# Kernel optimization log

Hardware: AMD Instinct MI355X
Metric: run time of the kernel (lower is better)

Reference implementation:

```python
import jax, jax.numpy as jnp
import numpy as np

E = 1024
H = 16
D = E // H  # head dim 64
B = 2
S = 2048


def setup_inputs() -> dict:
    key = jax.random.key(0)
    k1, k2, k3, k4, k5 = jax.random.split(key, 5)
    scale = 1.0 / np.sqrt(E)
    return {
        "x": jax.random.normal(k1, (B, S, E), dtype=jnp.float32),
        "W_in": jax.random.normal(k2, (E, 3 * E), dtype=jnp.float32) * scale,
        "b_in": jnp.zeros((3 * E,), dtype=jnp.float32),
        "W_out": jax.random.normal(k3, (E, E), dtype=jnp.float32) * scale,
        "b_out": jnp.zeros((E,), dtype=jnp.float32),
        "causal_mask": 1,
    }


def reference(x, W_in, b_in, W_out, b_out, causal_mask):
    b, s, e = x.shape
    qkv = x @ W_in + b_in                      # [B,S,3E]
    q, k, v = jnp.split(qkv, 3, axis=-1)
    # [B,S,E] -> [B,H,S,D]
    q = q.reshape(b, s, H, D).transpose(0, 2, 1, 3)
    k = k.reshape(b, s, H, D).transpose(0, 2, 1, 3)
    v = v.reshape(b, s, H, D).transpose(0, 2, 1, 3)
    scores = jnp.einsum("bhqd,bhkd->bhqk", q, k)
    if causal_mask:
        # mask applied before scaling in the original; -inf is scale-invariant
        mask = jnp.triu(jnp.ones((s, s), dtype=bool), k=1)
        scores = jnp.where(mask, -jnp.inf, scores)
    scores = scores / np.sqrt(D)
    weight = jax.nn.softmax(scores, axis=-1)
    out = jnp.einsum("bhqk,bhkd->bhqd", weight, v)   # [B,H,S,D]
    out = out.transpose(0, 2, 1, 3).reshape(b, s, e)
    return out @ W_out + b_out
```

## Files before the change

### kernel.cpp

```cpp
#include <hip/hip_runtime.h>
#include <hip/hip_bf16.h>
#include <cmath>

typedef __bf16 bf16;
typedef __attribute__((ext_vector_type(8))) __bf16 bf16x8;
typedef __attribute__((ext_vector_type(4))) __bf16 bf16x4;
typedef __attribute__((ext_vector_type(4))) float f32x4;
typedef __attribute__((ext_vector_type(16))) float f32x16;
typedef unsigned int u32;

constexpr int S  = 2048;
constexpr int E  = 1024;
constexpr int H  = 16;
constexpr int D  = 64;
constexpr int B  = 2;
constexpr int M  = B * S;
constexpr int N3 = 3 * E;
constexpr int NROWS = B * H * S;

__constant__ int P_tab_d[16] = {1,1,1,1,1,2,2,2,2,2,2,3,3,3,3,3};
__constant__ int S_tab_d[16] = {0,1,2,3,4,5,7,9,11,13,15,17,20,23,26,29};
__constant__ int c_ord_d[32] = {15,15,10,10, 15,14,14,14,13,9,9,4,
                                13,13,12,12,8,8, 12,11,11,11,7,7,3,
                                6,6, 5,5,2, 1, 0};
__constant__ int p_ord_d[32] = {1,2,0,1, 0,0,1,2,2,0,1,0,
                                0,1,1,2,0,1, 0,0,1,2,0,1,0,
                                0,1, 0,1,0, 0, 0};

static __device__ __forceinline__ void gload16(const void* g, void* l) {
  __builtin_amdgcn_global_load_lds((const __attribute__((address_space(1))) void*)g,
                                   (__attribute__((address_space(3))) void*)l, 16, 0, 0);
}

static __device__ __forceinline__ u32 pack2(float a, float b) {
  union { bf16 h[2]; u32 u; } r;
  r.h[0] = (bf16)a; r.h[1] = (bf16)b;
  return r.u;
}
typedef union { u32 w[4]; bf16x8 v; } FU;

__global__ __launch_bounds__(256) void k_prep(
    const float* __restrict__ x, bf16* __restrict__ xb,
    const float* __restrict__ W_in, bf16* __restrict__ wtin,
    const float* __restrict__ W_out, bf16* __restrict__ wtout)
{
  const int bid = blockIdx.x;
  if (bid < 4096) {
    const int i = (bid * 256 + threadIdx.x) * 4;
    const float4 v = *(const float4*)(x + i);
    bf16x4 o = { (bf16)v.x, (bf16)v.y, (bf16)v.z, (bf16)v.w };
    *(bf16x4*)(xb + i) = o;
  } else {
    __shared__ float t[32][33];
    const float* in;
    bf16* out;
    int R, C, bx, by;
    if (bid < 4096 + 3072) {
      const int b = bid - 4096;
      in = W_in; out = wtin; R = E; C = N3;
      bx = b % (N3 / 32); by = b / (N3 / 32);
    } else {
      const int b = bid - 4096 - 3072;
      in = W_out; out = wtout; R = E; C = E;
      bx = b % (E / 32); by = b / (E / 32);
    }
    const int c0 = bx * 32, r0 = by * 32;
    const int tx = threadIdx.x & 31, ty = threadIdx.x >> 5;
    #pragma unroll
    for (int j = 0; j < 32; j += 8)
      t[ty + j][tx] = in[(size_t)(r0 + ty + j) * C + c0 + tx];
    __syncthreads();
    #pragma unroll
    for (int j = 0; j < 32; j += 8)
      out[(size_t)(c0 + ty + j) * R + r0 + tx] = (bf16)t[tx][ty + j];
  }
}

template<int EPI>
__global__ __launch_bounds__(256) void k_gemm(
    const bf16* __restrict__ A, const bf16* __restrict__ Bt,
    const float* __restrict__ bias, float* __restrict__ outF,
    bf16* __restrict__ oQ, bf16* __restrict__ oK, bf16* __restrict__ oV,
    int Kdim, int Nn)
{
  __shared__ __align__(16) char smem[65536];
  const int tid = threadIdx.x;
  const int lane = tid & 63, w = tid >> 6;
  const int lane15 = lane & 15, quad = lane >> 4;
  const int wm = w >> 1, wn = w & 1;

  const int nbx = Nn >> 7;
  const int nwg = gridDim.x;
  const int bid = blockIdx.x;
  const int swz = (bid & 7) * (nwg >> 3) + (bid >> 3);
  const int bn0 = (swz % nbx) * 128;
  const int bm0 = (swz / nbx) * 128;

  const int so0 = w * 1024 + lane * 16;
  int srow[4], slk[4];
  #pragma unroll
  for (int p = 0; p < 4; ++p) {
    const int o = p * 4096 + so0;
    const int row = o >> 7, cbyte = o & 127;
    srow[p] = row;
    slk[p] = (cbyte ^ ((row & 7) << 4)) >> 1;
  }

  f32x4 acc[4][4] = {};
  const int nkt = Kdim >> 6;

  #pragma unroll
  for (int p = 0; p < 4; ++p) {
    gload16(A  + (size_t)(bm0 + srow[p]) * Kdim + slk[p], smem +         p * 4096 + w * 1024);
    gload16(Bt + (size_t)(bn0 + srow[p]) * Kdim + slk[p], smem + 32768 + p * 4096 + w * 1024);
  }

  #pragma unroll 1
  for (int kt = 0; kt < nkt; ++kt) {
    const int cur = kt & 1;
    __builtin_amdgcn_s_barrier();
    if (kt + 1 < nkt) {
      const int k0 = (kt + 1) << 6;
      const int nb = (cur ^ 1) * 16384;
      #pragma unroll
      for (int p = 0; p < 4; ++p) {
        gload16(A  + (size_t)(bm0 + srow[p]) * Kdim + k0 + slk[p],
                smem + nb +         p * 4096 + w * 1024);
        gload16(Bt + (size_t)(bn0 + srow[p]) * Kdim + k0 + slk[p],
                smem + nb + 32768 + p * 4096 + w * 1024);
      }
      asm volatile("s_waitcnt vmcnt(8)" ::: "memory");
    } else {
      asm volatile("s_waitcnt vmcnt(0)" ::: "memory");
    }
    __builtin_amdgcn_s_barrier();

    const char* cA = smem + cur * 16384;
    const char* cB = smem + 32768 + cur * 16384;
    #pragma unroll
    for (int kk = 0; kk < 2; ++kk) {
      bf16x8 af[4], bfr[4];
      #pragma unroll
      for (int f = 0; f < 4; ++f) {
        const int ra = wm * 64 + f * 16 + lane15;
        af[f] = *(const bf16x8*)(cA + ra * 128 +
                 ((kk * 64 + (quad << 4)) ^ ((ra & 7) << 4)));
        const int rb = wn * 64 + f * 16 + lane15;
        bfr[f] = *(const bf16x8*)(cB + rb * 128 +
                 ((kk * 64 + (quad << 4)) ^ ((rb & 7) << 4)));
      }
      #pragma unroll
      for (int i = 0; i < 4; ++i)
        #pragma unroll
        for (int j = 0; j < 4; ++j)
          acc[i][j] = __builtin_amdgcn_mfma_f32_16x16x32_bf16(af[i], bfr[j], acc[i][j], 0, 0, 0);
    }
  }

  if constexpr (EPI == 1) {
    #pragma unroll
    for (int i = 0; i < 4; ++i)
      #pragma unroll
      for (int j = 0; j < 4; ++j) {
        const int n = bn0 + wn * 64 + j * 16 + lane15;
        const float bv = bias[n];
        #pragma unroll
        for (int r = 0; r < 4; ++r) {
          const int m = bm0 + wm * 64 + i * 16 + quad * 4 + r;
          outF[(size_t)m * E + n] = acc[i][j][r] + bv;
        }
      }
  } else {
    const int which = bn0 >> 10;
    const int b  = bm0 >> 11;
    const int s0 = bm0 & (S - 1);
    const int cn0 = bn0 & (E - 1);
    if (which < 2) {
      __builtin_amdgcn_s_barrier();
      char* lC = smem;
      #pragma unroll
      for (int j = 0; j < 4; ++j) {
        const int n_loc = wn * 64 + j * 16 + lane15;
        const float bv = bias[bn0 + n_loc];
        #pragma unroll
        for (int i = 0; i < 4; ++i)
          #pragma unroll
          for (int r = 0; r < 4; ++r) {
            const int m_loc = wm * 64 + i * 16 + quad * 4 + r;
            *(bf16*)(lC + m_loc * 256 + ((n_loc * 2) ^ ((m_loc & 7) << 4))) =
                (bf16)(acc[i][j][r] + bv);
          }
      }
      __builtin_amdgcn_s_barrier();
      const int h0 = cn0 >> 6;
      #pragma unroll
      for (int it = 0; it < 8; ++it) {
        const int cch = w * 64 + it * 8 + (lane >> 3);
        const int m_loc = cch >> 1, hh = cch & 1, piece = lane & 7;
        const bf16x8 vv = *(const bf16x8*)(lC + m_loc * 256 +
                          ((hh * 128 + piece * 16) ^ ((m_loc & 7) << 4)));
        if (which == 0) {
          *(bf16x8*)(oQ + ((size_t)(b * H + h0 + hh) * S + s0 + m_loc) * D + piece * 8) = vv;
        } else {
          const size_t hb = (size_t)(b * H + h0 + hh) * S * D;
          const int tile = (s0 + m_loc) >> 6;
          const int row = m_loc & 63;
          *(bf16x8*)(oK + hb + (size_t)tile * 4096 + (piece >> 1) * 1024 +
                     (row >> 5) * 512 + (32 * (piece & 1) + (row & 31)) * 8) = vv;
        }
      }
    } else {
      #pragma unroll
      for (int j = 0; j < 4; ++j) {
        const int n_loc = wn * 64 + j * 16 + lane15;
        const int cn = cn0 + n_loc;
        const int hv = cn >> 6, dd = cn & 63;
        const float bv = bias[bn0 + n_loc];
        const size_t hb = (size_t)(b * H + hv) * S * D;
        #pragma unroll
        for (int i = 0; i < 4; ++i) {
          const int scol_g = s0 + wm * 64 + i * 16 + quad * 4;
          const int vtile = scol_g >> 6;
          const int cg = (scol_g & 63) >> 3;
          bf16x4 pk = { (bf16)(acc[i][j][0] + bv), (bf16)(acc[i][j][1] + bv),
                        (bf16)(acc[i][j][2] + bv), (bf16)(acc[i][j][3] + bv) };
          *(bf16x4*)(oV + hb + (size_t)vtile * 4096 + (cg >> 1) * 1024 +
                     (dd >> 5) * 512 + (32 * (cg & 1) + (dd & 31)) * 8 +
                     (quad & 1) * 4) = pk;
        }
      }
    }
  }
}

__global__ __launch_bounds__(256, 4) void k_attn(
    const bf16* __restrict__ Qb, const bf16* __restrict__ Kf, const bf16* __restrict__ Vf,
    bf16* __restrict__ pO0, bf16* __restrict__ pO1,
    float* __restrict__ pM, float* __restrict__ pL, const int* __restrict__ cmask)
{
  __shared__ float corr_lds[4][32];
  __shared__ float lrow_lds[4][32];

  const int tid = threadIdx.x, lane = tid & 63, w = tid >> 6;
  const int h = lane >> 5, q31 = lane & 31;
  const int bh = blockIdx.x;
  const int yy = blockIdx.y;
  const int c  = c_ord_d[yy];
  const int p  = p_ord_d[yy];
  const int Pc = P_tab_d[c];
  const int sslot = S_tab_d[c] + p;
  const int causal = cmask[0];
  const float S2 = 0.18033688011112042f;

  const bf16* Qh = Qb + (size_t)bh * S * D;
  const bf16* Kh = Kf + (size_t)bh * S * D;
  const bf16* Vh = Vf + (size_t)bh * S * D;

  const int nt = causal ? (2 * c + 2) : (S / 64);
  const int t0 = (p * nt) / Pc;
  const int t1 = ((p + 1) * nt) / Pc;
  const int q0w = c * 128 + 32 * w;
  const int qg  = q0w + q31;
  const int t1w = causal ? min(t1, ((q0w + 31) >> 6) + 1) : t1;

  bf16x8 qf[4];
  #pragma unroll
  for (int ds = 0; ds < 4; ++ds)
    qf[ds] = *(const bf16x8*)(Qh + (size_t)qg * D + 16 * ds + 8 * h);

  f32x16 o0 = {}, o1 = {};
  float mrun = -INFINITY, lr = 0.f;

  #pragma unroll 1
  for (int t = t0; t < t1w; ++t) {
    const bf16* ktb = Kh + (size_t)t * 4096;
    const bf16* vtb = Vh + (size_t)t * 4096;

    bf16x8 kf0[4], kf1[4];
    #pragma unroll
    for (int ds = 0; ds < 4; ++ds) {
      kf0[ds] = *(const bf16x8*)(ktb + ds * 1024 +       lane * 8);
      kf1[ds] = *(const bf16x8*)(ktb + ds * 1024 + 512 + lane * 8);
    }

    f32x16 s0v = {}, s1v = {};
    __builtin_amdgcn_s_setprio(1);
    #pragma unroll
    for (int ds = 0; ds < 4; ++ds) {
      s0v = __builtin_amdgcn_mfma_f32_32x32x16_bf16(kf0[ds], qf[ds], s0v, 0, 0, 0);
      s1v = __builtin_amdgcn_mfma_f32_32x32x16_bf16(kf1[ds], qf[ds], s1v, 0, 0, 0);
    }
    __builtin_amdgcn_s_setprio(0);

    if (causal && (64 * t + 63 > q0w)) {
      #pragma unroll
      for (int rr = 0; rr < 16; ++rr) {
        const int kg = 64 * t + (rr & 3) + 8 * (rr >> 2) + 4 * h;
        if (kg > qg)      s0v[rr] = -INFINITY;
        if (kg + 32 > qg) s1v[rr] = -INFINITY;
      }
    }

    float a8[8];
    #pragma unroll
    for (int i = 0; i < 8; ++i)
      a8[i] = fmaxf(fmaxf(s0v[i], s0v[i + 8]), fmaxf(s1v[i], s1v[i + 8]));
    float tmax = fmaxf(fmaxf(fmaxf(a8[0], a8[1]), fmaxf(a8[2], a8[3])),
                       fmaxf(fmaxf(a8[4], a8[5]), fmaxf(a8[6], a8[7])));
    tmax = fmaxf(tmax, __shfl_xor(tmax, 32, 64));

    const bool nogrow = __all(tmax <= mrun + 64.f);
    const float mnew = nogrow ? mrun : fmaxf(mrun, tmax);
    float corrf = 1.f;
    if (!nogrow) {
      corrf = __builtin_amdgcn_exp2f((mrun - mnew) * S2);
      corr_lds[w][q31] = corrf;
    }
    const float msc = mnew * S2;

    #pragma unroll
    for (int rr = 0; rr < 16; ++rr) {
      s0v[rr] = __builtin_amdgcn_exp2f(__builtin_fmaf(s0v[rr], S2, -msc));
      s1v[rr] = __builtin_amdgcn_exp2f(__builtin_fmaf(s1v[rr], S2, -msc));
    }

    float b8[8];
    #pragma unroll
    for (int i = 0; i < 8; ++i)
      b8[i] = (s0v[i] + s0v[i + 8]) + (s1v[i] + s1v[i + 8]);
    float psum = ((b8[0] + b8[1]) + (b8[2] + b8[3])) + ((b8[4] + b8[5]) + (b8[6] + b8[7]));
    psum += __shfl_xor(psum, 32, 64);
    lr = lr * corrf + psum;
    mrun = mnew;

    u32 pk[8][2];
    #pragma unroll
    for (int jj = 0; jj < 4; ++jj) {
      pk[jj][0]     = pack2(s0v[4 * jj],     s0v[4 * jj + 1]);
      pk[jj][1]     = pack2(s0v[4 * jj + 2], s0v[4 * jj + 3]);
      pk[jj + 4][0] = pack2(s1v[4 * jj],     s1v[4 * jj + 1]);
      pk[jj + 4][1] = pack2(s1v[4 * jj + 2], s1v[4 * jj + 3]);
    }

    if (!nogrow) {
      #pragma unroll
      for (int j = 0; j < 4; ++j) {
        const f32x4 cv = *(const f32x4*)&corr_lds[w][8 * j + 4 * h];
        #pragma unroll
        for (int sr = 0; sr < 4; ++sr) {
          o0[4 * j + sr] *= cv[sr];
          o1[4 * j + sr] *= cv[sr];
        }
      }
    }

    __builtin_amdgcn_s_setprio(1);
    #pragma unroll
    for (int ks = 0; ks < 4; ++ks) {
      u32 a0 = pk[2 * ks][0], b0 = pk[2 * ks + 1][0];
      u32 a1 = pk[2 * ks][1], b1 = pk[2 * ks + 1][1];
      asm volatile("v_permlane32_swap_b32 %0, %1" : "+v"(a0), "+v"(b0));
      asm volatile("v_permlane32_swap_b32 %0, %1" : "+v"(a1), "+v"(b1));
      FU f; f.w[0] = a0; f.w[1] = a1; f.w[2] = b0; f.w[3] = b1;
      const bf16x8 vf0 = *(const bf16x8*)(vtb + ks * 1024 +       lane * 8);
      const bf16x8 vf1 = *(const bf16x8*)(vtb + ks * 1024 + 512 + lane * 8);
      o0 = __builtin_amdgcn_mfma_f32_32x32x16_bf16(f.v, vf0, o0, 0, 0, 0);
      o1 = __builtin_amdgcn_mfma_f32_32x32x16_bf16(f.v, vf1, o1, 0, 0, 0);
    }
    __builtin_amdgcn_s_setprio(0);
  }

  const int slotbase = ((bh & 15) * 32 + sslot) * 128;
  if (h == 0) {
    pM[(size_t)(bh * 32 + sslot) * 128 + 32 * w + q31] = mrun;
    pL[(size_t)(bh * 32 + sslot) * 128 + 32 * w + q31] = lr;
  }
  lrow_lds[w][q31] = lr;
  bf16* po = (bh < 16 ? pO0 : pO1) + (size_t)slotbase * D;
  #pragma unroll
  for (int j = 0; j < 4; ++j) {
    const f32x4 lv = *(const f32x4*)&lrow_lds[w][8 * j + 4 * h];
    #pragma unroll
    for (int sr = 0; sr < 4; ++sr) {
      const int rr = 4 * j + sr;
      const float inv = lv[sr] > 0.f ? 1.0f / lv[sr] : 0.f;
      const int qloc = 32 * w + (rr & 3) + 8 * (rr >> 2) + 4 * h;
      bf16* dst = po + (size_t)qloc * D;
      dst[q31]      = (bf16)(o0[rr] * inv);
      dst[32 + q31] = (bf16)(o1[rr] * inv);
    }
  }
}

__global__ __launch_bounds__(256) void k_combine(
    const bf16* __restrict__ pO0, const bf16* __restrict__ pO1,
    const float* __restrict__ pM, const float* __restrict__ pL,
    bf16* __restrict__ AO)
{
  const float S2 = 0.18033688011112042f;
  const int idx = blockIdx.x * 256 + threadIdx.x;
  const int row = idx >> 3, d0 = (idx & 7) * 8;
  const int bh = row >> 11, s = row & 2047;
  const int c = s >> 7, local = s & 127;
  const int Pc = P_tab_d[c], Sc = S_tab_d[c];
  const bf16* pbase = (bh < 16 ? pO0 : pO1);

  float mv[3], lv[3];
  float m = -INFINITY;
  #pragma unroll
  for (int p = 0; p < 3; ++p) {
    if (p < Pc) {
      mv[p] = pM[(size_t)(bh * 32 + Sc + p) * 128 + local];
      lv[p] = pL[(size_t)(bh * 32 + Sc + p) * 128 + local];
      m = fmaxf(m, mv[p]);
    }
  }
  float wsum = 0.f, wv[3];
  #pragma unroll
  for (int p = 0; p < 3; ++p) {
    wv[p] = 0.f;
    if (p < Pc && lv[p] > 0.f) {
      wv[p] = lv[p] * __builtin_amdgcn_exp2f((mv[p] - m) * S2);
      wsum += wv[p];
    }
  }
  const float inv = 1.0f / wsum;
  float acc[8] = {};
  #pragma unroll
  for (int p = 0; p < 3; ++p) {
    if (p < Pc) {
      const bf16x8 a = *(const bf16x8*)(pbase +
          ((size_t)((bh & 15) * 32 + Sc + p) * 128 + local) * D + d0);
      #pragma unroll
      for (int i = 0; i < 8; ++i)
        acc[i] += wv[p] * (float)a[i];
    }
  }
  bf16x8 o;
  #pragma unroll
  for (int i = 0; i < 8; ++i)
    o[i] = (bf16)(acc[i] * inv);
  const int bb = row >> 15, hh = (row >> 11) & 15;
  *(bf16x8*)(AO + ((size_t)(bb * S + s)) * E + hh * D + d0) = o;
}

extern "C" void kernel_launch(void* const* d_in, const int* in_sizes, int n_in,
                              void* d_out, int out_size, void* d_ws, size_t ws_size,
                              hipStream_t stream) {
  (void)in_sizes; (void)n_in; (void)out_size; (void)ws_size;
  const float* x     = (const float*)d_in[0];
  const float* W_in  = (const float*)d_in[1];
  const float* b_in  = (const float*)d_in[2];
  const float* W_out = (const float*)d_in[3];
  const float* b_out = (const float*)d_in[4];
  const int*   cmask = (const int*)d_in[5];

  char* ws = (char*)d_ws;
  bf16* xb    = (bf16*)ws; ws += (size_t)M * E * 2;
  bf16* wtin  = (bf16*)ws; ws += (size_t)N3 * E * 2;
  bf16* wtout = (bf16*)ws; ws += (size_t)E * E * 2;
  bf16* qB    = (bf16*)ws; ws += (size_t)B * H * S * D * 2;
  bf16* kF    = (bf16*)ws; ws += (size_t)B * H * S * D * 2;
  bf16* vF    = (bf16*)ws; ws += (size_t)B * H * S * D * 2;
  bf16* ao    = (bf16*)ws; ws += (size_t)M * E * 2;
  bf16* pO1   = (bf16*)ws; ws += (size_t)NROWS * D * 2;
  float* pMb  = (float*)ws; ws += (size_t)2 * NROWS * 4;
  float* pLb  = (float*)ws; ws += (size_t)2 * NROWS * 4;
  bf16* pO0   = xb;

  k_prep<<<4096 + 3072 + 1024, 256, 0, stream>>>(x, xb, W_in, wtin, W_out, wtout);
  k_gemm<0><<<dim3((M / 128) * (N3 / 128)), 256, 0, stream>>>(
      xb, wtin, b_in, nullptr, qB, kF, vF, E, N3);
  k_attn<<<dim3(32, 32), 256, 0, stream>>>(qB, kF, vF, pO0, pO1, pMb, pLb, cmask);
  k_combine<<<NROWS * 8 / 256, 256, 0, stream>>>(pO0, pO1, pMb, pLb, ao);
  k_gemm<1><<<dim3((M / 128) * (E / 128)), 256, 0, stream>>>(
      ao, wtout, b_out, (float*)d_out, nullptr, nullptr, nullptr, E, E);
}
```

Measured before the change: 103.5 us.

## Split causal attention KV range into more partitions with a 40-slot schedule

Raises the per-query-chunk split-KV partition count to up to four and grows the attention grid from 32 to 40 slots per head, with a new greedy ordering table. The partial outputs get their own workspace buffer instead of reusing the x staging buffer, and the combine kernel merges up to four partials, skipping loads for zero-weight partitions. The aim is finer, more balanced work across CUs for the triangular causal workload, at the cost of more partial-output traffic and merge work.

```diff
diff --git a/kernel.cpp b/kernel.cpp
--- a/kernel.cpp
+++ b/kernel.cpp
@@ -17,15 +17,16 @@
 constexpr int M  = B * S;
 constexpr int N3 = 3 * E;
 constexpr int NROWS = B * H * S;
-
-__constant__ int P_tab_d[16] = {1,1,1,1,1,2,2,2,2,2,2,3,3,3,3,3};
-__constant__ int S_tab_d[16] = {0,1,2,3,4,5,7,9,11,13,15,17,20,23,26,29};
-__constant__ int c_ord_d[32] = {15,15,10,10, 15,14,14,14,13,9,9,4,
-                                13,13,12,12,8,8, 12,11,11,11,7,7,3,
-                                6,6, 5,5,2, 1, 0};
-__constant__ int p_ord_d[32] = {1,2,0,1, 0,0,1,2,2,0,1,0,
-                                0,1,1,2,0,1, 0,0,1,2,0,1,0,
-                                0,1, 0,1,0, 0, 0};
+constexpr int NSLOT = 40;
+
+__constant__ int P_tab_d[16] = {1,1,1,1,2,2,2,2,3,3,3,3,4,4,4,4};
+__constant__ int S_tab_d[16] = {0,1,2,3,4,6,8,10,12,15,18,21,24,28,32,36};
+__constant__ int c_ord_d[NSLOT] = {3,7,7,10,11,11,11,14,14,15,15,15,15,
+                                   6,6,9,9,10,10,12,12,13,13,13,13,14,14,
+                                   2,5,5,8,8,8,9,12,12, 4,4, 1, 0};
+__constant__ int p_ord_d[NSLOT] = {0,0,1,2,0,1,2,1,3,0,1,2,3,
+                                   0,1,1,2,0,1,1,3,0,1,2,3,0,2,
+                                   0,0,1,0,1,2,0,0,2, 0,1, 0, 0};
 
 static __device__ __forceinline__ void gload16(const void* g, void* l) {
   __builtin_amdgcn_global_load_lds((const __attribute__((address_space(1))) void*)g,
@@ -235,8 +236,8 @@
 
 __global__ __launch_bounds__(256, 4) void k_attn(
     const bf16* __restrict__ Qb, const bf16* __restrict__ Kf, const bf16* __restrict__ Vf,
-    bf16* __restrict__ pO0, bf16* __restrict__ pO1,
-    float* __restrict__ pM, float* __restrict__ pL, const int* __restrict__ cmask)
+    bf16* __restrict__ pO, float* __restrict__ pM, float* __restrict__ pL,
+    const int* __restrict__ cmask)
 {
   __shared__ float corr_lds[4][32];
   __shared__ float lrow_lds[4][32];
@@ -370,13 +371,13 @@
     __builtin_amdgcn_s_setprio(0);
   }
 
-  const int slotbase = ((bh & 15) * 32 + sslot) * 128;
+  const size_t slotbase = ((size_t)bh * NSLOT + sslot) * 128;
   if (h == 0) {
-    pM[(size_t)(bh * 32 + sslot) * 128 + 32 * w + q31] = mrun;
-    pL[(size_t)(bh * 32 + sslot) * 128 + 32 * w + q31] = lr;
+    pM[slotbase + 32 * w + q31] = mrun;
+    pL[slotbase + 32 * w + q31] = lr;
   }
   lrow_lds[w][q31] = lr;
-  bf16* po = (bh < 16 ? pO0 : pO1) + (size_t)slotbase * D;
+  bf16* po = pO + slotbase * D;
   #pragma unroll
   for (int j = 0; j < 4; ++j) {
     const f32x4 lv = *(const f32x4*)&lrow_lds[w][8 * j + 4 * h];
@@ -393,9 +394,8 @@
 }
 
 __global__ __launch_bounds__(256) void k_combine(
-    const bf16* __restrict__ pO0, const bf16* __restrict__ pO1,
-    const float* __restrict__ pM, const float* __restrict__ pL,
-    bf16* __restrict__ AO)
+    const bf16* __restrict__ pO, const float* __restrict__ pM,
+    const float* __restrict__ pL, bf16* __restrict__ AO)
 {
   const float S2 = 0.18033688011112042f;
   const int idx = blockIdx.x * 256 + threadIdx.x;
@@ -403,21 +403,20 @@
   const int bh = row >> 11, s = row & 2047;
   const int c = s >> 7, local = s & 127;
   const int Pc = P_tab_d[c], Sc = S_tab_d[c];
-  const bf16* pbase = (bh < 16 ? pO0 : pO1);
-
-  float mv[3], lv[3];
+
+  float mv[4], lv[4];
   float m = -INFINITY;
   #pragma unroll
-  for (int p = 0; p < 3; ++p) {
+  for (int p = 0; p < 4; ++p) {
     if (p < Pc) {
-      mv[p] = pM[(size_t)(bh * 32 + Sc + p) * 128 + local];
-      lv[p] = pL[(size_t)(bh * 32 + Sc + p) * 128 + local];
+      mv[p] = pM[((size_t)bh * NSLOT + Sc + p) * 128 + local];
+      lv[p] = pL[((size_t)bh * NSLOT + Sc + p) * 128 + local];
       m = fmaxf(m, mv[p]);
     }
   }
-  float wsum = 0.f, wv[3];
-  #pragma unroll
-  for (int p = 0; p < 3; ++p) {
+  float wsum = 0.f, wv[4];
+  #pragma unroll
+  for (int p = 0; p < 4; ++p) {
     wv[p] = 0.f;
     if (p < Pc && lv[p] > 0.f) {
       wv[p] = lv[p] * __builtin_amdgcn_exp2f((mv[p] - m) * S2);
@@ -427,10 +426,10 @@
   const float inv = 1.0f / wsum;
   float acc[8] = {};
   #pragma unroll
-  for (int p = 0; p < 3; ++p) {
-    if (p < Pc) {
-      const bf16x8 a = *(const bf16x8*)(pbase +
-          ((size_t)((bh & 15) * 32 + Sc + p) * 128 + local) * D + d0);
+  for (int p = 0; p < 4; ++p) {
+    if (p < Pc && wv[p] > 0.f) {
+      const bf16x8 a = *(const bf16x8*)(pO +
+          (((size_t)bh * NSLOT + Sc + p) * 128 + local) * D + d0);
       #pragma unroll
       for (int i = 0; i < 8; ++i)
         acc[i] += wv[p] * (float)a[i];
@@ -463,16 +462,15 @@
   bf16* kF    = (bf16*)ws; ws += (size_t)B * H * S * D * 2;
   bf16* vF    = (bf16*)ws; ws += (size_t)B * H * S * D * 2;
   bf16* ao    = (bf16*)ws; ws += (size_t)M * E * 2;
-  bf16* pO1   = (bf16*)ws; ws += (size_t)NROWS * D * 2;
-  float* pMb  = (float*)ws; ws += (size_t)2 * NROWS * 4;
-  float* pLb  = (float*)ws; ws += (size_t)2 * NROWS * 4;
-  bf16* pO0   = xb;
+  bf16* pO    = (bf16*)ws; ws += (size_t)32 * NSLOT * 128 * D * 2;
+  float* pMb  = (float*)ws; ws += (size_t)32 * NSLOT * 128 * 4;
+  float* pLb  = (float*)ws; ws += (size_t)32 * NSLOT * 128 * 4;
 
   k_prep<<<4096 + 3072 + 1024, 256, 0, stream>>>(x, xb, W_in, wtin, W_out, wtout);
   k_gemm<0><<<dim3((M / 128) * (N3 / 128)), 256, 0, stream>>>(
       xb, wtin, b_in, nullptr, qB, kF, vF, E, N3);
-  k_attn<<<dim3(32, 32), 256, 0, stream>>>(qB, kF, vF, pO0, pO1, pMb, pLb, cmask);
-  k_combine<<<NROWS * 8 / 256, 256, 0, stream>>>(pO0, pO1, pMb, pLb, ao);
+  k_attn<<<dim3(32, NSLOT), 256, 0, stream>>>(qB, kF, vF, pO, pMb, pLb, cmask);
+  k_combine<<<NROWS * 8 / 256, 256, 0, stream>>>(pO, pMb, pLb, ao);
   k_gemm<1><<<dim3((M / 128) * (E / 128)), 256, 0, stream>>>(
       ao, wtout, b_out, (float*)d_out, nullptr, nullptr, nullptr, E, E);
 }
```

New measurement: 108.3 us. 1.05x slower.
